# Optimization experiments

Measured on AMD Instinct MI355X. Metric: run time of the kernel, lower is better.

Reference implementation:

```python
import jax, jax.numpy as jnp
import numpy as np

N_NODES = 100000
N_EDGES = 1600000


def setup_inputs() -> dict:
    key = jax.random.key(0)
    k1, k2, k3, k4, k5, k6 = jax.random.split(key, 6)
    x = jax.random.normal(k1, (N_NODES, 2), dtype=jnp.float32)
    edge_index = jax.random.randint(k2, (2, N_EDGES), 0, N_NODES, dtype=jnp.int64)
    # Glorot-style init for GCN weights, zeros for biases (PyG defaults)
    W1 = jax.random.normal(k3, (2, 64), dtype=jnp.float32) * (1.0 / np.sqrt(2.0))
    b1 = jnp.zeros((64,), dtype=jnp.float32)
    W2 = jax.random.normal(k4, (64, 1), dtype=jnp.float32) * (1.0 / np.sqrt(64.0))
    b2 = jnp.zeros((1,), dtype=jnp.float32)
    return {"x": x, "edge_index": edge_index, "W1": W1, "b1": b1, "W2": W2, "b2": b2}


def reference(x, edge_index, W1, b1, W2, b2):
    N = x.shape[0]
    row, col = edge_index[0], edge_index[1]  # source, target (PyG flow source_to_target)
    # symmetric GCN normalization, degrees from target index (no self loops)
    deg = jax.ops.segment_sum(jnp.ones(edge_index.shape[1], x.dtype), col, num_segments=N)
    deg_inv_sqrt = jnp.where(deg > 0, jnp.where(deg > 0, deg, 1.0) ** -0.5, 0.0)
    norm = (deg_inv_sqrt[row] * deg_inv_sqrt[col])[:, None]  # [E,1]

    def gcn_conv(h, W, b):
        h = h @ W                       # [N,F_out] tiny GEMM
        msg = h[row] * norm             # gather + scale: [E,F_out]
        agg = jax.ops.segment_sum(msg, col, num_segments=N)  # scatter-add
        return agg + b

    h = jax.nn.relu(gcn_conv(x, W1, b1))   # dropout is identity in eval mode
    out = jax.nn.relu(gcn_conv(h, W2, b2))
    return out
```

## Files before the change

kernel.cpp:

```cpp
#include <hip/hip_runtime.h>
#include <math.h>

#define NN 100000
#define NE 1600000
#define BKT 448
#define NB 224
#define EPB 6400
#define NPB 250
#define STRIDE 9472
#define RT 1024

__device__ unsigned g_cursor[NB];

__global__ void __launch_bounds__(RT) reorder_kernel(
        const int* __restrict__ row, const int* __restrict__ col,
        unsigned* __restrict__ packed) {
    __shared__ int h[NB], lb[NB];
    __shared__ unsigned gaddr[NB], glim[NB];
    __shared__ int wsum[RT / 64];
    __shared__ uint2 sga[EPB];
    const int t = threadIdx.x;
    const int lane = t & 63, wid = t >> 6;
    const int e0 = blockIdx.x * EPB;

    for (int i = t; i < NB; i += RT) h[i] = 0;
    __syncthreads();

    const int4* rv = (const int4*)(row + e0);
    const int4* cv = (const int4*)(col + e0);
    unsigned pk[8]; int bb[8];
#pragma unroll
    for (int u = 0; u < 8; ++u) bb[u] = -1;
#pragma unroll
    for (int g = 0; g < 2; ++g) {
        int grp = g * RT + t;
        if (grp < EPB / 4) {
            int4 r4 = rv[grp], c4 = cv[grp];
            int rr[4] = {r4.x, r4.y, r4.z, r4.w};
            int cc[4] = {c4.x, c4.y, c4.z, c4.w};
#pragma unroll
            for (int j = 0; j < 4; ++j) {
                int b = cc[j] / BKT;
                int cl = cc[j] - b * BKT;
                pk[4 * g + j] = ((unsigned)rr[j] << 9) | (unsigned)cl;
                bb[4 * g + j] = b;
            }
        }
    }
#pragma unroll
    for (int u = 0; u < 8; ++u)
        if (bb[u] >= 0) atomicAdd(&h[bb[u]], 1);
    __syncthreads();

    int v = (t < NB) ? h[t] : 0;
    int incl = v;
#pragma unroll
    for (int d = 1; d < 64; d <<= 1) {
        int u2 = __shfl_up(incl, d);
        if (lane >= d) incl += u2;
    }
    if (lane == 63) wsum[wid] = incl;
    __syncthreads();
    int off = 0;
#pragma unroll
    for (int j = 0; j < 3; ++j)
        if (j < wid) off += wsum[j];
    if (t < NB) {
        lb[t] = off + incl - v;
        unsigned base = v ? atomicAdd(&g_cursor[t], (unsigned)v) : 0u;
        gaddr[t] = (unsigned)t * STRIDE + base;
        glim[t]  = (unsigned)(t + 1) * STRIDE;
    }
    __syncthreads();
    for (int i = t; i < NB; i += RT) h[i] = 0;
    __syncthreads();

#pragma unroll
    for (int u = 0; u < 8; ++u) {
        if (bb[u] >= 0) {
            int b = bb[u];
            int r = atomicAdd(&h[b], 1);
            unsigned a = gaddr[b] + (unsigned)r;
            if (a >= glim[b]) a = 0xFFFFFFFFu;
            sga[lb[b] + r] = make_uint2(pk[u], a);
        }
    }
    __syncthreads();
    for (int i = t; i < EPB; i += RT) {
        uint2 e = sga[i];
        if (e.y != 0xFFFFFFFFu) packed[e.y] = e.x;
    }
}

__global__ void __launch_bounds__(RT) sortb_kernel(
        const unsigned* __restrict__ packed, const float2* __restrict__ x2,
        unsigned* __restrict__ srow, int2* __restrict__ node_rng,
        float* __restrict__ dis, float2* __restrict__ y2) {
    __shared__ int cnt[BKT], rk[BKT], sexA[BKT];
    __shared__ int wsum[7];
    __shared__ unsigned srt[STRIDE];
    __shared__ int sLp;
    const int t = threadIdx.x;
    const int lane = t & 63, wid = t >> 6;
    const int b = blockIdx.x;
    const int s0 = b * STRIDE;
    const int L = min((int)g_cursor[b], STRIDE);
    if (t == 0) { sLp = 0; g_cursor[b] = 0u; }
    const int L4 = L >> 2;

    for (int i = t; i < BKT; i += RT) { cnt[i] = 0; rk[i] = 0; }
    __syncthreads();

    const uint4* pv4 = (const uint4*)(packed + s0);
    for (int g = t; g < L4; g += RT) {
        uint4 p4 = pv4[g];
        atomicAdd(&cnt[p4.x & 511u], 1);
        atomicAdd(&cnt[p4.y & 511u], 1);
        atomicAdd(&cnt[p4.z & 511u], 1);
        atomicAdd(&cnt[p4.w & 511u], 1);
    }
    for (int i = 4 * L4 + t; i < L; i += RT)
        atomicAdd(&cnt[packed[s0 + i] & 511u], 1);
    __syncthreads();

    int v = (t < BKT) ? cnt[t] : 0;
    int vp = (v + 3) & ~3;
    int incl = vp;
#pragma unroll
    for (int d = 1; d < 64; d <<= 1) {
        int u2 = __shfl_up(incl, d);
        if (lane >= d) incl += u2;
    }
    if (lane == 63 && wid < 7) wsum[wid] = incl;
    __syncthreads();
    int off = 0;
#pragma unroll
    for (int j = 0; j < 6; ++j)
        if (j < wid) off += wsum[j];
    if (t < BKT) {
        int sex = off + incl - vp;
        if (sex + v > STRIDE) v = max(0, STRIDE - sex);
        sexA[t] = sex;
        if (v > 0) atomicMax(&sLp, sex + ((v + 3) & ~3));
        int node = b * BKT + t;
        if (node < NN) {
            float dv = (v > 0) ? rsqrtf((float)v) : 0.0f;
            dis[node] = dv;
            float2 xv = x2[node];
            y2[node] = make_float2(xv.x * dv, xv.y * dv);
            node_rng[node] = make_int2(s0 + sex, s0 + sex + v);
        }
    }
    __syncthreads();

    for (int g = t; g < L4; g += RT) {
        uint4 p4 = pv4[g];
        unsigned pp[4] = {p4.x, p4.y, p4.z, p4.w};
#pragma unroll
        for (int j = 0; j < 4; ++j) {
            int cl = pp[j] & 511u;
            int r = atomicAdd(&rk[cl], 1);
            int idx = sexA[cl] + r;
            if (idx < STRIDE) srt[idx] = pp[j] >> 9;
        }
    }
    for (int i = 4 * L4 + t; i < L; i += RT) {
        unsigned p = packed[s0 + i];
        int cl = p & 511u;
        int r = atomicAdd(&rk[cl], 1);
        int idx = sexA[cl] + r;
        if (idx < STRIDE) srt[idx] = p >> 9;
    }
    __syncthreads();
    const int Lp4 = sLp >> 2;
    uint4* so4 = (uint4*)(srow + s0);
    for (int g = t; g < Lp4; g += RT) so4[g] = ((const uint4*)srt)[g];
}

__global__ void conv1_kernel(const unsigned* __restrict__ srow, const int2* __restrict__ node_rng,
                             const float2* __restrict__ y2, const float* __restrict__ dis,
                             const float* __restrict__ W1, const float* __restrict__ b1,
                             const float* __restrict__ W2, float* __restrict__ z2) {
    __shared__ float sW0[64], sW1[64], sb1[64], sW2[64];
    int t = threadIdx.x;
    if (t < 64) { sW0[t] = W1[t]; sW1[t] = W1[64 + t]; sb1[t] = b1[t]; sW2[t] = W2[t]; }
    __syncthreads();
    int lane = t & 3;
    int node = blockIdx.x * 64 + (t >> 2);
    if (node >= NN) return;
    int2 rng = node_rng[node];
    int v = rng.y - rng.x;
    const uint4* s4 = (const uint4*)(srow + rng.x);
    float sx = 0.f, sy = 0.f;
    for (int g = lane; 4 * g < v; g += 4) {
        uint4 i4 = s4[g];
        unsigned ii[4] = {i4.x, i4.y, i4.z, i4.w};
#pragma unroll
        for (int j = 0; j < 4; ++j) {
            if (4 * g + j < v) {
                float2 vy = y2[ii[j]];
                sx += vy.x; sy += vy.y;
            }
        }
    }
    sx += __shfl_xor(sx, 1); sy += __shfl_xor(sy, 1);
    sx += __shfl_xor(sx, 2); sy += __shfl_xor(sy, 2);
    float dv = dis[node];
    float a0 = sx * dv, a1 = sy * dv;
    float acc = 0.0f;
    int j0 = lane * 16;
#pragma unroll
    for (int jj = 0; jj < 16; ++jj) {
        int j = j0 + jj;
        float h = fmaf(a0, sW0[j], fmaf(a1, sW1[j], sb1[j]));
        acc = fmaf(fmaxf(h, 0.0f), sW2[j], acc);
    }
    acc += __shfl_xor(acc, 1);
    acc += __shfl_xor(acc, 2);
    if (lane == 0) z2[node] = acc * dv;
}

__global__ void conv2_kernel(const unsigned* __restrict__ srow, const int2* __restrict__ node_rng,
                             const float* __restrict__ z2, const float* __restrict__ dis,
                             const float* __restrict__ b2, float* __restrict__ out) {
    int t = threadIdx.x;
    int lane = t & 3;
    int node = blockIdx.x * 64 + (t >> 2);
    if (node >= NN) return;
    int2 rng = node_rng[node];
    int v = rng.y - rng.x;
    const uint4* s4 = (const uint4*)(srow + rng.x);
    float s = 0.f;
    for (int g = lane; 4 * g < v; g += 4) {
        uint4 i4 = s4[g];
        unsigned ii[4] = {i4.x, i4.y, i4.z, i4.w};
#pragma unroll
        for (int j = 0; j < 4; ++j)
            if (4 * g + j < v) s += z2[ii[j]];
    }
    s += __shfl_xor(s, 1);
    s += __shfl_xor(s, 2);
    if (lane == 0)
        out[node] = fmaxf(fmaf(dis[node], s, b2[0]), 0.0f);
}

extern "C" void kernel_launch(void* const* d_in, const int* in_sizes, int n_in,
                              void* d_out, int out_size, void* d_ws, size_t ws_size,
                              hipStream_t stream) {
    const float* x  = (const float*)d_in[0];
    const int*   ei = (const int*)d_in[1];
    const float* W1 = (const float*)d_in[2];
    const float* b1 = (const float*)d_in[3];
    const float* W2 = (const float*)d_in[4];
    const float* b2 = (const float*)d_in[5];
    float* out = (float*)d_out;

    const int* row = ei;
    const int* col = ei + NE;

    unsigned* packed   = (unsigned*)d_ws;
    unsigned* srow     = packed + (size_t)NB * STRIDE;
    float2*   y2       = (float2*)(srow + (size_t)NB * STRIDE);
    float*    dis      = (float*)(y2 + NN);
    float*    z2       = dis + NN;
    int2*     node_rng = (int2*)(z2 + NN);

    reorder_kernel<<<NPB, RT, 0, stream>>>(row, col, packed);
    sortb_kernel  <<<NB, RT, 0, stream>>>(packed, (const float2*)x,
                                          srow, node_rng, dis, y2);
    conv1_kernel  <<<(NN + 63) / 64, 256, 0, stream>>>(srow, node_rng, y2, dis,
                                                       W1, b1, W2, z2);
    conv2_kernel  <<<(NN + 63) / 64, 256, 0, stream>>>(srow, node_rng, z2, dis, b2, out);
}
```

Measured before the change: 114.1 us.

## Fuse reorder, bucket sort and both GCN convs into one cooperative kernel

Replaces the four separate launches with a single cooperative persistent kernel of 224 blocks that uses grid-wide syncs between phases. Each block keeps its sorted neighbor list in shared memory, so the srow, node_rng and dis global arrays and their writes and reads go away. Edges per block are enlarged so 224 blocks cover all edges. The cost is three grid barriers and only 224 blocks doing the gather phases, which limits occupancy and latency hiding for the random y2/z2 gathers.

```diff
diff --git a/kernel.cpp b/kernel.cpp
--- a/kernel.cpp
+++ b/kernel.cpp
@@ -1,274 +1,283 @@
 #include <hip/hip_runtime.h>
+#include <hip/hip_cooperative_groups.h>
 #include <math.h>
+
+namespace cg = cooperative_groups;
 
 #define NN 100000
 #define NE 1600000
 #define BKT 448
 #define NB 224
-#define EPB 6400
-#define NPB 250
-#define STRIDE 9472
+#define EPB 7168
+#define STRIDE 8960
 #define RT 1024
 
 __device__ unsigned g_cursor[NB];
 
-__global__ void __launch_bounds__(RT) reorder_kernel(
-        const int* __restrict__ row, const int* __restrict__ col,
-        unsigned* __restrict__ packed) {
-    __shared__ int h[NB], lb[NB];
-    __shared__ unsigned gaddr[NB], glim[NB];
-    __shared__ int wsum[RT / 64];
-    __shared__ uint2 sga[EPB];
+struct SA {
+    int h[NB], lb[NB];
+    unsigned gaddr[NB], glim[NB];
+    int wsum[16];
+    uint2 sga[EPB];
+};
+struct SP {
+    unsigned srt[STRIDE];
+    int cnt[BKT], rk[BKT], sexA[BKT], vA[BKT];
+    int wsum[7];
+    float w0[64], w1[64], wb[64], w2[64];
+};
+union SMem { SA a; SP p; };
+
+__global__ void __launch_bounds__(RT, 1) gcn_mega(
+        const float2* __restrict__ x2, const int* __restrict__ ei,
+        const float* __restrict__ W1, const float* __restrict__ b1,
+        const float* __restrict__ W2, const float* __restrict__ b2,
+        float* __restrict__ out,
+        unsigned* __restrict__ packed, float2* __restrict__ y2,
+        float* __restrict__ z2)
+{
+    cg::grid_group grid = cg::this_grid();
+    __shared__ SMem sm;
     const int t = threadIdx.x;
     const int lane = t & 63, wid = t >> 6;
-    const int e0 = blockIdx.x * EPB;
-
-    for (int i = t; i < NB; i += RT) h[i] = 0;
-    __syncthreads();
-
-    const int4* rv = (const int4*)(row + e0);
-    const int4* cv = (const int4*)(col + e0);
-    unsigned pk[8]; int bb[8];
-#pragma unroll
-    for (int u = 0; u < 8; ++u) bb[u] = -1;
-#pragma unroll
-    for (int g = 0; g < 2; ++g) {
-        int grp = g * RT + t;
-        if (grp < EPB / 4) {
-            int4 r4 = rv[grp], c4 = cv[grp];
-            int rr[4] = {r4.x, r4.y, r4.z, r4.w};
-            int cc[4] = {c4.x, c4.y, c4.z, c4.w};
+    const int blk = blockIdx.x;
+    const int* row = ei;
+    const int* col = ei + NE;
+
+    {
+        for (int i = t; i < NB; i += RT) sm.a.h[i] = 0;
+        __syncthreads();
+
+        const int e0 = blk * EPB;
+        const int n = min(EPB, NE - e0);
+        const int n4 = n >> 2;
+        const int4* rv = (const int4*)(row + e0);
+        const int4* cv = (const int4*)(col + e0);
+        unsigned pk[8]; int bb[8];
+#pragma unroll
+        for (int u = 0; u < 8; ++u) bb[u] = -1;
+#pragma unroll
+        for (int g = 0; g < 2; ++g) {
+            int grp = g * RT + t;
+            if (grp < n4) {
+                int4 r4 = rv[grp], c4 = cv[grp];
+                int rr[4] = {r4.x, r4.y, r4.z, r4.w};
+                int cc[4] = {c4.x, c4.y, c4.z, c4.w};
+#pragma unroll
+                for (int j = 0; j < 4; ++j) {
+                    int b = cc[j] / BKT;
+                    int cl = cc[j] - b * BKT;
+                    pk[4 * g + j] = ((unsigned)rr[j] << 9) | (unsigned)cl;
+                    bb[4 * g + j] = b;
+                }
+            }
+        }
+#pragma unroll
+        for (int u = 0; u < 8; ++u)
+            if (bb[u] >= 0) atomicAdd(&sm.a.h[bb[u]], 1);
+        __syncthreads();
+
+        int v = (t < NB) ? sm.a.h[t] : 0;
+        int incl = v;
+#pragma unroll
+        for (int d = 1; d < 64; d <<= 1) {
+            int u2 = __shfl_up(incl, d);
+            if (lane >= d) incl += u2;
+        }
+        if (lane == 63) sm.a.wsum[wid] = incl;
+        __syncthreads();
+        int off = 0;
+#pragma unroll
+        for (int j = 0; j < 3; ++j)
+            if (j < wid) off += sm.a.wsum[j];
+        if (t < NB) {
+            sm.a.lb[t] = off + incl - v;
+            unsigned base = v ? atomicAdd(&g_cursor[t], (unsigned)v) : 0u;
+            sm.a.gaddr[t] = (unsigned)t * STRIDE + base;
+            sm.a.glim[t]  = (unsigned)(t + 1) * STRIDE;
+        }
+        __syncthreads();
+        for (int i = t; i < NB; i += RT) sm.a.h[i] = 0;
+        __syncthreads();
+
+#pragma unroll
+        for (int u = 0; u < 8; ++u) {
+            if (bb[u] >= 0) {
+                int b = bb[u];
+                int r = atomicAdd(&sm.a.h[b], 1);
+                unsigned a = sm.a.gaddr[b] + (unsigned)r;
+                if (a >= sm.a.glim[b]) a = 0xFFFFFFFFu;
+                sm.a.sga[sm.a.lb[b] + r] = make_uint2(pk[u], a);
+            }
+        }
+        __syncthreads();
+        for (int i = t; i < n; i += RT) {
+            uint2 e = sm.a.sga[i];
+            if (e.y != 0xFFFFFFFFu) packed[e.y] = e.x;
+        }
+    }
+    grid.sync();
+
+    const int b = blk;
+    const int s0 = b * STRIDE;
+    {
+        const int L = min((int)g_cursor[b], STRIDE);
+        const int L4 = L >> 2;
+        for (int i = t; i < BKT; i += RT) { sm.p.cnt[i] = 0; sm.p.rk[i] = 0; }
+        if (t >= 512 && t < 576) {
+            int j = t - 512;
+            sm.p.w0[j] = W1[j]; sm.p.w1[j] = W1[64 + j];
+            sm.p.wb[j] = b1[j]; sm.p.w2[j] = W2[j];
+        }
+        __syncthreads();
+        if (t == 0) g_cursor[b] = 0u;
+
+        const uint4* pv4 = (const uint4*)(packed + s0);
+        for (int g = t; g < L4; g += RT) {
+            uint4 p4 = pv4[g];
+            atomicAdd(&sm.p.cnt[p4.x & 511u], 1);
+            atomicAdd(&sm.p.cnt[p4.y & 511u], 1);
+            atomicAdd(&sm.p.cnt[p4.z & 511u], 1);
+            atomicAdd(&sm.p.cnt[p4.w & 511u], 1);
+        }
+        for (int i = 4 * L4 + t; i < L; i += RT)
+            atomicAdd(&sm.p.cnt[packed[s0 + i] & 511u], 1);
+        __syncthreads();
+
+        int v = (t < BKT) ? sm.p.cnt[t] : 0;
+        int vp = (v + 3) & ~3;
+        int incl = vp;
+#pragma unroll
+        for (int d = 1; d < 64; d <<= 1) {
+            int u2 = __shfl_up(incl, d);
+            if (lane >= d) incl += u2;
+        }
+        if (lane == 63 && wid < 7) sm.p.wsum[wid] = incl;
+        __syncthreads();
+        int off = 0;
+#pragma unroll
+        for (int j = 0; j < 6; ++j)
+            if (j < wid) off += sm.p.wsum[j];
+        if (t < BKT) {
+            int sex = off + incl - vp;
+            if (sex + v > STRIDE) v = max(0, STRIDE - sex);
+            sm.p.sexA[t] = sex;
+            sm.p.vA[t] = v;
+            int node = b * BKT + t;
+            if (node < NN) {
+                float dv = (v > 0) ? rsqrtf((float)v) : 0.0f;
+                float2 xv = x2[node];
+                y2[node] = make_float2(xv.x * dv, xv.y * dv);
+            }
+        }
+        __syncthreads();
+
+        for (int g = t; g < L4; g += RT) {
+            uint4 p4 = pv4[g];
+            unsigned pp[4] = {p4.x, p4.y, p4.z, p4.w};
 #pragma unroll
             for (int j = 0; j < 4; ++j) {
-                int b = cc[j] / BKT;
-                int cl = cc[j] - b * BKT;
-                pk[4 * g + j] = ((unsigned)rr[j] << 9) | (unsigned)cl;
-                bb[4 * g + j] = b;
-            }
-        }
-    }
-#pragma unroll
-    for (int u = 0; u < 8; ++u)
-        if (bb[u] >= 0) atomicAdd(&h[bb[u]], 1);
-    __syncthreads();
-
-    int v = (t < NB) ? h[t] : 0;
-    int incl = v;
-#pragma unroll
-    for (int d = 1; d < 64; d <<= 1) {
-        int u2 = __shfl_up(incl, d);
-        if (lane >= d) incl += u2;
-    }
-    if (lane == 63) wsum[wid] = incl;
-    __syncthreads();
-    int off = 0;
-#pragma unroll
-    for (int j = 0; j < 3; ++j)
-        if (j < wid) off += wsum[j];
-    if (t < NB) {
-        lb[t] = off + incl - v;
-        unsigned base = v ? atomicAdd(&g_cursor[t], (unsigned)v) : 0u;
-        gaddr[t] = (unsigned)t * STRIDE + base;
-        glim[t]  = (unsigned)(t + 1) * STRIDE;
-    }
-    __syncthreads();
-    for (int i = t; i < NB; i += RT) h[i] = 0;
-    __syncthreads();
-
-#pragma unroll
-    for (int u = 0; u < 8; ++u) {
-        if (bb[u] >= 0) {
-            int b = bb[u];
-            int r = atomicAdd(&h[b], 1);
-            unsigned a = gaddr[b] + (unsigned)r;
-            if (a >= glim[b]) a = 0xFFFFFFFFu;
-            sga[lb[b] + r] = make_uint2(pk[u], a);
-        }
-    }
-    __syncthreads();
-    for (int i = t; i < EPB; i += RT) {
-        uint2 e = sga[i];
-        if (e.y != 0xFFFFFFFFu) packed[e.y] = e.x;
-    }
-}
-
-__global__ void __launch_bounds__(RT) sortb_kernel(
-        const unsigned* __restrict__ packed, const float2* __restrict__ x2,
-        unsigned* __restrict__ srow, int2* __restrict__ node_rng,
-        float* __restrict__ dis, float2* __restrict__ y2) {
-    __shared__ int cnt[BKT], rk[BKT], sexA[BKT];
-    __shared__ int wsum[7];
-    __shared__ unsigned srt[STRIDE];
-    __shared__ int sLp;
-    const int t = threadIdx.x;
-    const int lane = t & 63, wid = t >> 6;
-    const int b = blockIdx.x;
-    const int s0 = b * STRIDE;
-    const int L = min((int)g_cursor[b], STRIDE);
-    if (t == 0) { sLp = 0; g_cursor[b] = 0u; }
-    const int L4 = L >> 2;
-
-    for (int i = t; i < BKT; i += RT) { cnt[i] = 0; rk[i] = 0; }
-    __syncthreads();
-
-    const uint4* pv4 = (const uint4*)(packed + s0);
-    for (int g = t; g < L4; g += RT) {
-        uint4 p4 = pv4[g];
-        atomicAdd(&cnt[p4.x & 511u], 1);
-        atomicAdd(&cnt[p4.y & 511u], 1);
-        atomicAdd(&cnt[p4.z & 511u], 1);
-        atomicAdd(&cnt[p4.w & 511u], 1);
-    }
-    for (int i = 4 * L4 + t; i < L; i += RT)
-        atomicAdd(&cnt[packed[s0 + i] & 511u], 1);
-    __syncthreads();
-
-    int v = (t < BKT) ? cnt[t] : 0;
-    int vp = (v + 3) & ~3;
-    int incl = vp;
-#pragma unroll
-    for (int d = 1; d < 64; d <<= 1) {
-        int u2 = __shfl_up(incl, d);
-        if (lane >= d) incl += u2;
-    }
-    if (lane == 63 && wid < 7) wsum[wid] = incl;
-    __syncthreads();
-    int off = 0;
-#pragma unroll
-    for (int j = 0; j < 6; ++j)
-        if (j < wid) off += wsum[j];
-    if (t < BKT) {
-        int sex = off + incl - vp;
-        if (sex + v > STRIDE) v = max(0, STRIDE - sex);
-        sexA[t] = sex;
-        if (v > 0) atomicMax(&sLp, sex + ((v + 3) & ~3));
-        int node = b * BKT + t;
-        if (node < NN) {
+                int cl = pp[j] & 511u;
+                int r = atomicAdd(&sm.p.rk[cl], 1);
+                int idx = sm.p.sexA[cl] + r;
+                if (idx < STRIDE) sm.p.srt[idx] = pp[j] >> 9;
+            }
+        }
+        for (int i = 4 * L4 + t; i < L; i += RT) {
+            unsigned p = packed[s0 + i];
+            int cl = p & 511u;
+            int r = atomicAdd(&sm.p.rk[cl], 1);
+            int idx = sm.p.sexA[cl] + r;
+            if (idx < STRIDE) sm.p.srt[idx] = p >> 9;
+        }
+    }
+    grid.sync();
+
+    {
+        const int qlane = t & 3;
+        const int q = t >> 2;
+        for (int nd = q; nd < BKT; nd += RT / 4) {
+            int node = b * BKT + nd;
+            if (node >= NN) break;
+            int v = sm.p.vA[nd];
+            const uint4* s4 = (const uint4*)(sm.p.srt + sm.p.sexA[nd]);
+            float sx = 0.f, sy = 0.f;
+            for (int g = qlane; 4 * g < v; g += 4) {
+                uint4 i4 = s4[g];
+                unsigned ii[4] = {i4.x, i4.y, i4.z, i4.w};
+#pragma unroll
+                for (int j = 0; j < 4; ++j) {
+                    if (4 * g + j < v) {
+                        float2 vy = y2[ii[j]];
+                        sx += vy.x; sy += vy.y;
+                    }
+                }
+            }
+            sx += __shfl_xor(sx, 1); sy += __shfl_xor(sy, 1);
+            sx += __shfl_xor(sx, 2); sy += __shfl_xor(sy, 2);
             float dv = (v > 0) ? rsqrtf((float)v) : 0.0f;
-            dis[node] = dv;
-            float2 xv = x2[node];
-            y2[node] = make_float2(xv.x * dv, xv.y * dv);
-            node_rng[node] = make_int2(s0 + sex, s0 + sex + v);
-        }
-    }
-    __syncthreads();
-
-    for (int g = t; g < L4; g += RT) {
-        uint4 p4 = pv4[g];
-        unsigned pp[4] = {p4.x, p4.y, p4.z, p4.w};
-#pragma unroll
-        for (int j = 0; j < 4; ++j) {
-            int cl = pp[j] & 511u;
-            int r = atomicAdd(&rk[cl], 1);
-            int idx = sexA[cl] + r;
-            if (idx < STRIDE) srt[idx] = pp[j] >> 9;
-        }
-    }
-    for (int i = 4 * L4 + t; i < L; i += RT) {
-        unsigned p = packed[s0 + i];
-        int cl = p & 511u;
-        int r = atomicAdd(&rk[cl], 1);
-        int idx = sexA[cl] + r;
-        if (idx < STRIDE) srt[idx] = p >> 9;
-    }
-    __syncthreads();
-    const int Lp4 = sLp >> 2;
-    uint4* so4 = (uint4*)(srow + s0);
-    for (int g = t; g < Lp4; g += RT) so4[g] = ((const uint4*)srt)[g];
-}
-
-__global__ void conv1_kernel(const unsigned* __restrict__ srow, const int2* __restrict__ node_rng,
-                             const float2* __restrict__ y2, const float* __restrict__ dis,
-                             const float* __restrict__ W1, const float* __restrict__ b1,
-                             const float* __restrict__ W2, float* __restrict__ z2) {
-    __shared__ float sW0[64], sW1[64], sb1[64], sW2[64];
-    int t = threadIdx.x;
-    if (t < 64) { sW0[t] = W1[t]; sW1[t] = W1[64 + t]; sb1[t] = b1[t]; sW2[t] = W2[t]; }
-    __syncthreads();
-    int lane = t & 3;
-    int node = blockIdx.x * 64 + (t >> 2);
-    if (node >= NN) return;
-    int2 rng = node_rng[node];
-    int v = rng.y - rng.x;
-    const uint4* s4 = (const uint4*)(srow + rng.x);
-    float sx = 0.f, sy = 0.f;
-    for (int g = lane; 4 * g < v; g += 4) {
-        uint4 i4 = s4[g];
-        unsigned ii[4] = {i4.x, i4.y, i4.z, i4.w};
-#pragma unroll
-        for (int j = 0; j < 4; ++j) {
-            if (4 * g + j < v) {
-                float2 vy = y2[ii[j]];
-                sx += vy.x; sy += vy.y;
-            }
-        }
-    }
-    sx += __shfl_xor(sx, 1); sy += __shfl_xor(sy, 1);
-    sx += __shfl_xor(sx, 2); sy += __shfl_xor(sy, 2);
-    float dv = dis[node];
-    float a0 = sx * dv, a1 = sy * dv;
-    float acc = 0.0f;
-    int j0 = lane * 16;
-#pragma unroll
-    for (int jj = 0; jj < 16; ++jj) {
-        int j = j0 + jj;
-        float h = fmaf(a0, sW0[j], fmaf(a1, sW1[j], sb1[j]));
-        acc = fmaf(fmaxf(h, 0.0f), sW2[j], acc);
-    }
-    acc += __shfl_xor(acc, 1);
-    acc += __shfl_xor(acc, 2);
-    if (lane == 0) z2[node] = acc * dv;
-}
-
-__global__ void conv2_kernel(const unsigned* __restrict__ srow, const int2* __restrict__ node_rng,
-                             const float* __restrict__ z2, const float* __restrict__ dis,
-                             const float* __restrict__ b2, float* __restrict__ out) {
-    int t = threadIdx.x;
-    int lane = t & 3;
-    int node = blockIdx.x * 64 + (t >> 2);
-    if (node >= NN) return;
-    int2 rng = node_rng[node];
-    int v = rng.y - rng.x;
-    const uint4* s4 = (const uint4*)(srow + rng.x);
-    float s = 0.f;
-    for (int g = lane; 4 * g < v; g += 4) {
-        uint4 i4 = s4[g];
-        unsigned ii[4] = {i4.x, i4.y, i4.z, i4.w};
-#pragma unroll
-        for (int j = 0; j < 4; ++j)
-            if (4 * g + j < v) s += z2[ii[j]];
-    }
-    s += __shfl_xor(s, 1);
-    s += __shfl_xor(s, 2);
-    if (lane == 0)
-        out[node] = fmaxf(fmaf(dis[node], s, b2[0]), 0.0f);
+            float a0 = sx * dv, a1 = sy * dv;
+            float acc = 0.0f;
+            const int j0 = qlane * 16;
+#pragma unroll
+            for (int jj = 0; jj < 16; ++jj) {
+                int j = j0 + jj;
+                float h = fmaf(a0, sm.p.w0[j], fmaf(a1, sm.p.w1[j], sm.p.wb[j]));
+                acc = fmaf(fmaxf(h, 0.0f), sm.p.w2[j], acc);
+            }
+            acc += __shfl_xor(acc, 1);
+            acc += __shfl_xor(acc, 2);
+            if (qlane == 0) z2[node] = acc * dv;
+        }
+    }
+    grid.sync();
+
+    {
+        const int qlane = t & 3;
+        const int q = t >> 2;
+        const float bias = b2[0];
+        for (int nd = q; nd < BKT; nd += RT / 4) {
+            int node = b * BKT + nd;
+            if (node >= NN) break;
+            int v = sm.p.vA[nd];
+            const uint4* s4 = (const uint4*)(sm.p.srt + sm.p.sexA[nd]);
+            float s = 0.f;
+            for (int g = qlane; 4 * g < v; g += 4) {
+                uint4 i4 = s4[g];
+                unsigned ii[4] = {i4.x, i4.y, i4.z, i4.w};
+#pragma unroll
+                for (int j = 0; j < 4; ++j)
+                    if (4 * g + j < v) s += z2[ii[j]];
+            }
+            s += __shfl_xor(s, 1);
+            s += __shfl_xor(s, 2);
+            if (qlane == 0) {
+                float dv = (v > 0) ? rsqrtf((float)v) : 0.0f;
+                out[node] = fmaxf(fmaf(dv, s, bias), 0.0f);
+            }
+        }
+    }
 }
 
 extern "C" void kernel_launch(void* const* d_in, const int* in_sizes, int n_in,
                               void* d_out, int out_size, void* d_ws, size_t ws_size,
                               hipStream_t stream) {
-    const float* x  = (const float*)d_in[0];
-    const int*   ei = (const int*)d_in[1];
-    const float* W1 = (const float*)d_in[2];
-    const float* b1 = (const float*)d_in[3];
-    const float* W2 = (const float*)d_in[4];
-    const float* b2 = (const float*)d_in[5];
+    const float2* x2 = (const float2*)d_in[0];
+    const int*    ei = (const int*)d_in[1];
+    const float*  W1 = (const float*)d_in[2];
+    const float*  b1 = (const float*)d_in[3];
+    const float*  W2 = (const float*)d_in[4];
+    const float*  b2 = (const float*)d_in[5];
     float* out = (float*)d_out;
 
-    const int* row = ei;
-    const int* col = ei + NE;
-
-    unsigned* packed   = (unsigned*)d_ws;
-    unsigned* srow     = packed + (size_t)NB * STRIDE;
-    float2*   y2       = (float2*)(srow + (size_t)NB * STRIDE);
-    float*    dis      = (float*)(y2 + NN);
-    float*    z2       = dis + NN;
-    int2*     node_rng = (int2*)(z2 + NN);
-
-    reorder_kernel<<<NPB, RT, 0, stream>>>(row, col, packed);
-    sortb_kernel  <<<NB, RT, 0, stream>>>(packed, (const float2*)x,
-                                          srow, node_rng, dis, y2);
-    conv1_kernel  <<<(NN + 63) / 64, 256, 0, stream>>>(srow, node_rng, y2, dis,
-                                                       W1, b1, W2, z2);
-    conv2_kernel  <<<(NN + 63) / 64, 256, 0, stream>>>(srow, node_rng, z2, dis, b2, out);
+    unsigned* packed = (unsigned*)d_ws;
+    float2*   y2     = (float2*)(packed + (size_t)NB * STRIDE);
+    float*    z2     = (float*)(y2 + NN);
+
+    void* args[] = {
+        (void*)&x2, (void*)&ei, (void*)&W1, (void*)&b1, (void*)&W2, (void*)&b2,
+        (void*)&out, (void*)&packed, (void*)&y2, (void*)&z2
+    };
+    hipLaunchCooperativeKernel((const void*)gcn_mega, dim3(NB), dim3(RT),
+                               args, 0, stream);
 }
```

Measured after the change: 199.1 us. +74.4%, slower.
